# Kernel tuning notes

Hardware: AMD Instinct MI355X
Metric: run time of the kernel (lower is better)

## Reference

```python
import jax, jax.numpy as jnp
import numpy as np
from jax import lax

WIN = 7            # win_size -> (7,7,7) window in 3d mode
NPIX = WIN ** 3    # 343
K1, K2 = 0.01, 0.03
COV_NORM = NPIX / (NPIX - 1)
DN = ('NCDHW', 'OIDHW', 'NCDHW')


def _box3d(x):
    """Separable uniform (box) mean filter, VALID padding. Same math as
    conv3d with a ones(wt,ws,ws)/NPIX kernel, but O(win) per voxel per axis."""
    kd = jnp.ones((1, 1, WIN, 1, 1), x.dtype)
    kh = jnp.ones((1, 1, 1, WIN, 1), x.dtype)
    kw = jnp.ones((1, 1, 1, 1, WIN), x.dtype)
    x = lax.conv_general_dilated(x, kd, (1, 1, 1), 'VALID', dimension_numbers=DN)
    x = lax.conv_general_dilated(x, kh, (1, 1, 1), 'VALID', dimension_numbers=DN)
    x = lax.conv_general_dilated(x, kw, (1, 1, 1), 'VALID', dimension_numbers=DN)
    return x / NPIX


def setup_inputs() -> dict:
    key = jax.random.key(0)
    k1, k2, k3 = jax.random.split(key, 3)
    shape = (4, 1, 32, 320, 320)  # [B, C=1, T, H, W]
    pred = jax.random.normal(k1, shape, dtype=jnp.float32)
    targ = jax.random.normal(k2, shape, dtype=jnp.float32)
    data_range = jax.random.uniform(k3, (4,), dtype=jnp.float32)
    return {'pred': pred, 'targ': targ, 'data_range': data_range}


def reference(pred, targ, data_range):
    dr = data_range[:, None, None, None, None].astype(pred.dtype)
    C1 = (K1 * dr) ** 2
    C2 = (K2 * dr) ** 2
    ux = _box3d(pred)
    uy = _box3d(targ)
    uxx = _box3d(pred * pred)
    uyy = _box3d(targ * targ)
    uxy = _box3d(pred * targ)
    vx = COV_NORM * (uxx - ux * ux)
    vy = COV_NORM * (uyy - uy * uy)
    vxy = COV_NORM * (uxy - ux * uy)
    A1 = 2 * ux * uy + C1
    A2 = 2 * vxy + C2
    B1 = ux ** 2 + uy ** 2 + C1
    B2 = vx + vy + C2
    S = (A1 * A2) / (B1 * B2)
    return (1 - S).mean()
```

## Files before the change

### kernel.cpp

```cpp
#include <hip/hip_runtime.h>


#define WIN 7
#define NPIX 343

constexpr int B = 4, T = 32, H = 320, W = 320;
constexpr int TO = T - 6, HO = H - 6, WO = W - 6;
constexpr long long NOUT = (long long)B * TO * HO * WO;

constexpr int TH = 16, TW = 32;
constexpr int IH = 22;
constexpr int SPW = 44;
constexpr int CW  = 41;
constexpr int C2W = 24;
constexpr int NTH = 20, NTW = 10;
constexpr int OT_PER = 13, NS = OT_PER + 6;

__global__ __launch_bounds__(256) void ssim3d_fused(
    const float* __restrict__ pred,
    const float* __restrict__ targ,
    const float* __restrict__ drange,
    double* __restrict__ acc)
{
    __shared__ float sp[2][IH][SPW];
    __shared__ float sq[2][IH][SPW];
    __shared__ float col [2][4][TH][CW];
    __shared__ float col2[2][4][TH][C2W];
    __shared__ float wsum[4];

    const int bx   = blockIdx.x;
    const int b    = bx / (2 * NTH * NTW);
    int rem        = bx % (2 * NTH * NTW);
    const int half = rem / (NTH * NTW);
    rem            = rem % (NTH * NTW);
    const int h0   = (rem / NTW) * TH;
    const int w0   = (rem % NTW) * TW;
    const int t0   = half * OT_PER;

    const int tid = threadIdx.x;

    const float* pb = pred + (long long)b * T * H * W;
    const float* qb = targ + (long long)b * T * H * W;

    const int item0 = tid;
    const int f0s = item0 / 220, rm0 = item0 % 220;
    const int r0s = rm0 / 10, c0s = rm0 % 10;
    const int gr0 = min(h0 + r0s, H - 1), gc0 = min(w0 + 4 * c0s, W - 4);
    const float* gb0 = (f0s ? qb : pb) + (long long)gr0 * W + gc0;
    const int o0 = r0s * SPW + 4 * c0s;

    const bool act1 = (tid < 184);
    const int item1 = 256 + tid;
    const int f1s = item1 / 220, rm1 = item1 % 220;
    const int r1s = rm1 / 10, c1s = rm1 % 10;
    const int gr1 = min(h0 + r1s, H - 1), gc1 = min(w0 + 4 * c1s, W - 4);
    const float* gb1 = (f1s ? qb : pb) + (long long)gr1 * W + gc1;
    const int o1 = r1s * SPW + 4 * c1s;

    float4 pr0, pr1;
    auto prefetchw = [&](int s) {
        const long long so = (long long)(t0 + s) * H * W;
        pr0 = *reinterpret_cast<const float4*>(gb0 + so);
        if (act1) pr1 = *reinterpret_cast<const float4*>(gb1 + so);
    };
    auto commitw = [&](int buf) {
        float* d0 = (f0s ? &sq[buf][0][0] : &sp[buf][0][0]) + o0;
        *reinterpret_cast<float4*>(d0) = pr0;
        if (act1) {
            float* d1 = (f1s ? &sq[buf][0][0] : &sp[buf][0][0]) + o1;
            *reinterpret_cast<float4*>(d1) = pr1;
        }
    };

    const bool colw = (tid < 152);
    const int rp = tid / 19, cpi = tid % 19;
    const int cr0 = 2 * rp;
    const int cc  = 2 * cpi;

    const int oh = tid >> 4, k = tid & 15;
    const bool vh = (h0 + oh < HO);
    const bool vE = vh && (w0 + 2 * k     < WO);
    const bool vO = vh && (w0 + 2 * k + 1 < WO);

    const float dr  = drange[b];
    const float C1v = (0.01f * dr) * (0.01f * dr);
    const float C2v = (0.03f * dr) * (0.03f * dr);
    const float inv  = 1.0f / (float)NPIX;
    const float covn = (float)NPIX / (float)(NPIX - 1);

    float rE[4][7], rO[4][7], tE[4], tO[4];
#pragma unroll
    for (int f = 0; f < 4; ++f) {
        tE[f] = tO[f] = 0.f;
#pragma unroll
        for (int j = 0; j < 7; ++j) { rE[f][j] = rO[f][j] = 0.f; }
    }
    float loss = 0.f;

    auto ssim1 = [&](const float* tt) {
        float ux  = tt[0] * inv, uy = tt[1] * inv;
        float u2  = tt[2] * inv, uxy = tt[3] * inv;
        float B2 = covn * (u2 - ux * ux - uy * uy) + C2v;
        float A2 = 2.f * covn * (uxy - ux * uy) + C2v;
        float A1 = 2.f * ux * uy + C1v;
        float B1 = ux * ux + uy * uy + C1v;
        return 1.f - (A1 * A2) / (B1 * B2);
    };

    prefetchw(0);
    commitw(0);
    prefetchw(1);
    __syncthreads();

    for (int a = 0; a < 21; a += 7) {
#pragma unroll
        for (int jj = 0; jj < 7; ++jj) {
            const int s = a + jj;
            if (s < NS) {
                const int bs = s & 1, bn = bs ^ 1;

                if (s + 1 < NS) commitw(bn);

                if (colw) {
                    float2 mid[4], row0[4], row7[4];
#pragma unroll
                    for (int dy = 0; dy < 8; ++dy) {
                        float2 p = *reinterpret_cast<const float2*>(&sp[bs][cr0 + dy][cc]);
                        float2 q = *reinterpret_cast<const float2*>(&sq[bs][cr0 + dy][cc]);
                        float2 v[4];
                        v[0] = p;
                        v[1] = q;
                        v[2] = make_float2(fmaf(p.x, p.x, q.x * q.x),
                                           fmaf(p.y, p.y, q.y * q.y));
                        v[3] = make_float2(p.x * q.x, p.y * q.y);
                        if (dy == 0) {
#pragma unroll
                            for (int f = 0; f < 4; ++f) row0[f] = v[f];
                        } else if (dy == 7) {
#pragma unroll
                            for (int f = 0; f < 4; ++f) row7[f] = v[f];
                        } else if (dy == 1) {
#pragma unroll
                            for (int f = 0; f < 4; ++f) mid[f] = v[f];
                        } else {
#pragma unroll
                            for (int f = 0; f < 4; ++f) {
                                mid[f].x += v[f].x; mid[f].y += v[f].y;
                            }
                        }
                    }
#pragma unroll
                    for (int f = 0; f < 4; ++f) {
                        float ax = row0[f].x + mid[f].x;
                        float ay = row0[f].y + mid[f].y;
                        float bxv = mid[f].x + row7[f].x;
                        float byv = mid[f].y + row7[f].y;
                        col[bs][f][cr0][cc]       = ax;
                        col[bs][f][cr0][cc + 1]   = ay;
                        col[bs][f][cr0 + 1][cc]     = bxv;
                        col[bs][f][cr0 + 1][cc + 1] = byv;
                        col2[bs][f][cr0][cpi]     = ax + ay;
                        col2[bs][f][cr0 + 1][cpi] = bxv + byv;
                    }
                }

                if (s + 2 < NS) prefetchw(s + 2);

                __syncthreads();

                float sEv[4], sOv[4];
#pragma unroll
                for (int f = 0; f < 4; ++f) {
                    const float* c2r = &col2[bs][f][oh][0];
                    float s8 = c2r[k] + c2r[k + 1] + c2r[k + 2] + c2r[k + 3];
                    const float* cr = &col[bs][f][oh][0];
                    sEv[f] = s8 - cr[2 * k + 7];
                    sOv[f] = s8 - cr[2 * k];
                }
#pragma unroll
                for (int f = 0; f < 4; ++f) {
                    tE[f] += sEv[f] - rE[f][jj];  rE[f][jj] = sEv[f];
                    tO[f] += sOv[f] - rO[f][jj];  rO[f][jj] = sOv[f];
                }

                if (s >= 6) {
                    if (vE) loss += ssim1(tE);
                    if (vO) loss += ssim1(tO);
                }
            }
        }
    }

    for (int off = 32; off > 0; off >>= 1)
        loss += __shfl_down(loss, off, 64);
    const int lane = tid & 63;
    const int wid  = tid >> 6;
    if (lane == 0) wsum[wid] = loss;
    __syncthreads();
    if (tid == 0) {
        float s = wsum[0] + wsum[1] + wsum[2] + wsum[3];
        atomicAdd(acc, (double)s);
    }
}

__global__ void ssim3d_finalize(const double* __restrict__ acc,
                                float* __restrict__ out)
{
    out[0] = (float)(acc[0] / (double)NOUT);
}

extern "C" void kernel_launch(void* const* d_in, const int* in_sizes, int n_in,
                              void* d_out, int out_size, void* d_ws, size_t ws_size,
                              hipStream_t stream)
{
    const float* pred   = (const float*)d_in[0];
    const float* targ   = (const float*)d_in[1];
    const float* drange = (const float*)d_in[2];
    float* out  = (float*)d_out;
    double* acc = (double*)d_ws;

    hipMemsetAsync(acc, 0, sizeof(double), stream);

    const int nblocks = B * 2 * NTH * NTW;
    ssim3d_fused<<<nblocks, 256, 0, stream>>>(pred, targ, drange, acc);
    ssim3d_finalize<<<1, 1, 0, stream>>>(acc, out);
}
```

Baseline: 85.40 us.

## Transpose column-sum shared buffer and drop pair-sum array; use fast divide

Stores the vertical column sums in a transposed layout (column-major by output column, with rows contiguous) written as float2, and remaps column-stage threads so consecutive threads cover consecutive row pairs. The separate pairwise-sum array is removed, and the horizontal 7-tap sum is read directly as 7 strided loads plus one extra load for the odd output. This cuts shared-memory writes and footprint and is meant to reduce bank conflicts. In exchange the horizontal stage does more LDS reads per output. The SSIM division is also replaced with __fdividef, which slightly reduces precision.

Result: slower. 94.47 us (+10.6%).

```diff
diff --git a/kernel.cpp b/kernel.cpp
--- a/kernel.cpp
+++ b/kernel.cpp
@@ -11,8 +11,8 @@
 constexpr int TH = 16, TW = 32;
 constexpr int IH = 22;
 constexpr int SPW = 44;
-constexpr int CW  = 41;
-constexpr int C2W = 24;
+constexpr int NCOL = 38;
+constexpr int CRW  = 18;
 constexpr int NTH = 20, NTW = 10;
 constexpr int OT_PER = 13, NS = OT_PER + 6;
 
@@ -24,8 +24,7 @@
 {
     __shared__ float sp[2][IH][SPW];
     __shared__ float sq[2][IH][SPW];
-    __shared__ float col [2][4][TH][CW];
-    __shared__ float col2[2][4][TH][C2W];
+    __shared__ float colT[2][4][NCOL][CRW];
     __shared__ float wsum[4];
 
     const int bx   = blockIdx.x;
@@ -42,8 +41,7 @@
     const float* pb = pred + (long long)b * T * H * W;
     const float* qb = targ + (long long)b * T * H * W;
 
-    const int item0 = tid;
-    const int f0s = item0 / 220, rm0 = item0 % 220;
+    const int f0s = tid / 220, rm0 = tid % 220;
     const int r0s = rm0 / 10, c0s = rm0 % 10;
     const int gr0 = min(h0 + r0s, H - 1), gc0 = min(w0 + 4 * c0s, W - 4);
     const float* gb0 = (f0s ? qb : pb) + (long long)gr0 * W + gc0;
@@ -73,7 +71,8 @@
     };
 
     const bool colw = (tid < 152);
-    const int rp = tid / 19, cpi = tid % 19;
+    const int rp  = tid & 7;
+    const int cpi = tid >> 3;
     const int cr0 = 2 * rp;
     const int cc  = 2 * cpi;
 
@@ -104,7 +103,7 @@
         float A2 = 2.f * covn * (uxy - ux * uy) + C2v;
         float A1 = 2.f * ux * uy + C1v;
         float B1 = ux * ux + uy * uy + C1v;
-        return 1.f - (A1 * A2) / (B1 * B2);
+        return 1.f - __fdividef(A1 * A2, B1 * B2);
     };
 
     prefetchw(0);
@@ -151,16 +150,12 @@
                     }
 #pragma unroll
                     for (int f = 0; f < 4; ++f) {
-                        float ax = row0[f].x + mid[f].x;
-                        float ay = row0[f].y + mid[f].y;
+                        float ax  = row0[f].x + mid[f].x;
+                        float ay  = row0[f].y + mid[f].y;
                         float bxv = mid[f].x + row7[f].x;
                         float byv = mid[f].y + row7[f].y;
-                        col[bs][f][cr0][cc]       = ax;
-                        col[bs][f][cr0][cc + 1]   = ay;
-                        col[bs][f][cr0 + 1][cc]     = bxv;
-                        col[bs][f][cr0 + 1][cc + 1] = byv;
-                        col2[bs][f][cr0][cpi]     = ax + ay;
-                        col2[bs][f][cr0 + 1][cpi] = bxv + byv;
+                        *reinterpret_cast<float2*>(&colT[bs][f][cc][cr0])     = make_float2(ax, bxv);
+                        *reinterpret_cast<float2*>(&colT[bs][f][cc + 1][cr0]) = make_float2(ay, byv);
                     }
                 }
 
@@ -171,11 +166,12 @@
                 float sEv[4], sOv[4];
 #pragma unroll
                 for (int f = 0; f < 4; ++f) {
-                    const float* c2r = &col2[bs][f][oh][0];
-                    float s8 = c2r[k] + c2r[k + 1] + c2r[k + 2] + c2r[k + 3];
-                    const float* cr = &col[bs][f][oh][0];
-                    sEv[f] = s8 - cr[2 * k + 7];
-                    sOv[f] = s8 - cr[2 * k];
+                    const float* cf = &colT[bs][f][0][0] + 2 * k * CRW + oh;
+                    float c0 = cf[0];
+                    float s7 = c0 + cf[CRW] + cf[2*CRW] + cf[3*CRW]
+                                  + cf[4*CRW] + cf[5*CRW] + cf[6*CRW];
+                    sEv[f] = s7;
+                    sOv[f] = s7 - c0 + cf[7*CRW];
                 }
 #pragma unroll
                 for (int f = 0; f < 4; ++f) {
```

## Deepen global prefetch to two slices ahead and swizzle blocks across XCDs

Applied to the files above, without the earlier changes.

Global loads now run three slices ahead of compute instead of two, using two register sets that alternate with the shared-memory buffer index. This hides more of the global memory latency per time step. The block index is also remapped so consecutive launch IDs, which the hardware spreads round-robin over the 8 XCDs, cover contiguous spatial tiles on each XCD for better L2 locality. The extra register set raises register pressure.

Result: slower. 107.5 us (+25.9%).

```diff
diff --git a/kernel.cpp b/kernel.cpp
--- a/kernel.cpp
+++ b/kernel.cpp
@@ -15,6 +15,8 @@
 constexpr int C2W = 24;
 constexpr int NTH = 20, NTW = 10;
 constexpr int OT_PER = 13, NS = OT_PER + 6;
+constexpr int NBLK = B * 2 * NTH * NTW;
+constexpr int CPX  = NBLK / 8;
 
 __global__ __launch_bounds__(256) void ssim3d_fused(
     const float* __restrict__ pred,
@@ -28,7 +30,9 @@
     __shared__ float col2[2][4][TH][C2W];
     __shared__ float wsum[4];
 
-    const int bx   = blockIdx.x;
+    const int bid = blockIdx.x;
+    const int bx  = (bid & 7) * CPX + (bid >> 3);
+
     const int b    = bx / (2 * NTH * NTW);
     int rem        = bx % (2 * NTH * NTW);
     const int half = rem / (NTH * NTW);
@@ -42,8 +46,7 @@
     const float* pb = pred + (long long)b * T * H * W;
     const float* qb = targ + (long long)b * T * H * W;
 
-    const int item0 = tid;
-    const int f0s = item0 / 220, rm0 = item0 % 220;
+    const int f0s = tid / 220, rm0 = tid % 220;
     const int r0s = rm0 / 10, c0s = rm0 % 10;
     const int gr0 = min(h0 + r0s, H - 1), gc0 = min(w0 + 4 * c0s, W - 4);
     const float* gb0 = (f0s ? qb : pb) + (long long)gr0 * W + gc0;
@@ -57,18 +60,26 @@
     const float* gb1 = (f1s ? qb : pb) + (long long)gr1 * W + gc1;
     const int o1 = r1s * SPW + 4 * c1s;
 
-    float4 pr0, pr1;
-    auto prefetchw = [&](int s) {
+    float4 prA0, prA1, prB0, prB1;
+    auto prefetchw = [&](int s, int set) {
         const long long so = (long long)(t0 + s) * H * W;
-        pr0 = *reinterpret_cast<const float4*>(gb0 + so);
-        if (act1) pr1 = *reinterpret_cast<const float4*>(gb1 + so);
+        if (set == 0) {
+            prA0 = *reinterpret_cast<const float4*>(gb0 + so);
+            if (act1) prA1 = *reinterpret_cast<const float4*>(gb1 + so);
+        } else {
+            prB0 = *reinterpret_cast<const float4*>(gb0 + so);
+            if (act1) prB1 = *reinterpret_cast<const float4*>(gb1 + so);
+        }
     };
-    auto commitw = [&](int buf) {
+    auto commitw = [&](int buf, int set) {
         float* d0 = (f0s ? &sq[buf][0][0] : &sp[buf][0][0]) + o0;
-        *reinterpret_cast<float4*>(d0) = pr0;
-        if (act1) {
-            float* d1 = (f1s ? &sq[buf][0][0] : &sp[buf][0][0]) + o1;
-            *reinterpret_cast<float4*>(d1) = pr1;
+        float* d1 = (f1s ? &sq[buf][0][0] : &sp[buf][0][0]) + o1;
+        if (set == 0) {
+            *reinterpret_cast<float4*>(d0) = prA0;
+            if (act1) *reinterpret_cast<float4*>(d1) = prA1;
+        } else {
+            *reinterpret_cast<float4*>(d0) = prB0;
+            if (act1) *reinterpret_cast<float4*>(d1) = prB1;
         }
     };
 
@@ -107,9 +118,10 @@
         return 1.f - (A1 * A2) / (B1 * B2);
     };
 
-    prefetchw(0);
-    commitw(0);
-    prefetchw(1);
+    prefetchw(0, 0);
+    prefetchw(1, 1);
+    commitw(0, 0);
+    prefetchw(2, 0);
     __syncthreads();
 
     for (int a = 0; a < 21; a += 7) {
@@ -119,7 +131,7 @@
             if (s < NS) {
                 const int bs = s & 1, bn = bs ^ 1;
 
-                if (s + 1 < NS) commitw(bn);
+                if (s + 1 < NS) commitw(bn, bn);
 
                 if (colw) {
                     float2 mid[4], row0[4], row7[4];
@@ -151,12 +163,12 @@
                     }
 #pragma unroll
                     for (int f = 0; f < 4; ++f) {
-                        float ax = row0[f].x + mid[f].x;
-                        float ay = row0[f].y + mid[f].y;
+                        float ax  = row0[f].x + mid[f].x;
+                        float ay  = row0[f].y + mid[f].y;
                         float bxv = mid[f].x + row7[f].x;
                         float byv = mid[f].y + row7[f].y;
-                        col[bs][f][cr0][cc]       = ax;
-                        col[bs][f][cr0][cc + 1]   = ay;
+                        col[bs][f][cr0][cc]         = ax;
+                        col[bs][f][cr0][cc + 1]     = ay;
                         col[bs][f][cr0 + 1][cc]     = bxv;
                         col[bs][f][cr0 + 1][cc + 1] = byv;
                         col2[bs][f][cr0][cpi]     = ax + ay;
@@ -164,7 +176,7 @@
                     }
                 }
 
-                if (s + 2 < NS) prefetchw(s + 2);
+                if (s + 3 < NS) prefetchw(s + 3, bn);
 
                 __syncthreads();
 
@@ -221,7 +233,6 @@
 
     hipMemsetAsync(acc, 0, sizeof(double), stream);
 
-    const int nblocks = B * 2 * NTH * NTW;
-    ssim3d_fused<<<nblocks, 256, 0, stream>>>(pred, targ, drange, acc);
+    ssim3d_fused<<<NBLK, 256, 0, stream>>>(pred, targ, drange, acc);
     ssim3d_finalize<<<1, 1, 0, stream>>>(acc, out);
 }
```
